# Optimization experiments

Measured on AMD Instinct MI355X. Metric: run time of the kernel, lower is better.

The kernel has to match this reference:

```python
import jax, jax.numpy as jnp
import numpy as np

B = 131072     # batch of observations
OBS = 17       # HalfCheetah-v5 obs dim
ACT = 6        # HalfCheetah-v5 action dim
M = 16         # number of charts / experts
HID = 256      # encoder / value hidden width (hardcoded in module)
GHID = 128     # gate hidden width (hardcoded)
R = 24.0       # chart radius in whitened feature space
BETA = 1.0     # locality prior strength
NEG = -1e9     # masked-logit fill (finite to keep grads clean)
LOG_STD_MIN, LOG_STD_MAX = -20.0, 2.0


def setup_inputs() -> dict:
    key = jax.random.key(0)
    ks = jax.random.split(key, 12)
    def rn(i, shape, sc):
        return jax.random.normal(ks[i], shape, dtype=jnp.float32) * sc
    return {
        "obs": jax.random.normal(ks[0], (B, OBS), dtype=jnp.float32),
        # encoder MLP (only the two hidden tanh layers feed the feature 'feat')
        "W1": rn(1, (OBS, HID), 0.2), "b1": jnp.zeros((HID,), jnp.float32),
        "W2": rn(2, (HID, HID), 0.06), "b2": jnp.zeros((HID,), jnp.float32),
        # gate: Linear(256,128) -> tanh -> Linear(128,m)
        "Wg1": rn(3, (HID, GHID), 0.06), "bg1": jnp.zeros((GHID,), jnp.float32),
        "Wg2": rn(4, (GHID, M), 0.1), "bg2": jnp.zeros((M,), jnp.float32),
        # m local Gaussian heads: mu Linear(256, act), shared log_std param per head
        "muW": rn(5, (M, HID, ACT), 0.06), "mub": jnp.zeros((M, ACT), jnp.float32),
        "log_std": jnp.zeros((M, ACT), jnp.float32),
        # value head: 256 -> 256 -> 256 -> 1 with tanh
        "Wv1": rn(6, (HID, HID), 0.06), "bv1": jnp.zeros((HID,), jnp.float32),
        "Wv2": rn(7, (HID, HID), 0.06), "bv2": jnp.zeros((HID,), jnp.float32),
        "Wv3": rn(8, (HID, 1), 0.06), "bv3": jnp.zeros((1,), jnp.float32),
        # chart cover state (frozen params in the torch module)
        "centers": jax.random.normal(ks[9], (M, HID), dtype=jnp.float32),
        "stats_mean": jnp.zeros((HID,), jnp.float32),
        "stats_var": jnp.ones((HID,), jnp.float32),
    }


def reference(obs, W1, b1, W2, b2, Wg1, bg1, Wg2, bg2, muW, mub, log_std,
              Wv1, bv1, Wv2, bv2, Wv3, bv3, centers, stats_mean, stats_var):
    # shared encoder phi(o): two tanh layers -> feat [B, HID]
    feat = jnp.tanh(jnp.tanh(obs @ W1 + b1) @ W2 + b2)

    # whitened features and squared distances to chart centers (cdist via gram trick)
    zw = (feat - stats_mean) / jnp.sqrt(stats_var + 1e-6)          # [B, HID]
    d2 = jnp.maximum(
        jnp.sum(zw * zw, axis=-1, keepdims=True)
        + jnp.sum(centers * centers, axis=-1)
        - 2.0 * (zw @ centers.T), 0.0)                              # [B, M]
    dists = jnp.sqrt(d2)

    # gate logits + locality prior -beta * ||z - c_i||^2 / r^2
    logits = jnp.tanh(feat @ Wg1 + bg1) @ Wg2 + bg2 - BETA * d2 / (R * R)

    # masked softmax restricted to active charts; nearest chart always active
    active = dists <= R
    nearest = jax.nn.one_hot(jnp.argmin(dists, axis=1), M, dtype=bool)
    active = active | nearest
    g = jax.nn.softmax(jnp.where(active, logits, NEG), axis=1)      # [B, M]

    # local expert heads mu_i(z), then convex combination of mu and log_std
    mus = jnp.einsum('bd,mda->bma', feat, muW) + mub                # [B, M, ACT]
    mu_bar = jnp.einsum('bm,bma->ba', g, mus)                       # [B, ACT]
    s_bar = jnp.clip(g @ log_std, LOG_STD_MIN, LOG_STD_MAX)         # [B, ACT]

    # value head on shared features
    v = (jnp.tanh(jnp.tanh(feat @ Wv1 + bv1) @ Wv2 + bv2) @ Wv3 + bv3)[:, 0]
    return mu_bar, s_bar, v
```

## Files before the change

kernel.cpp:

```cpp
#include <hip/hip_runtime.h>
#include <hip/hip_bf16.h>

#define BDIM 512
#define TB 64
#define OBS_D 17
#define HID 256
#define GHID 128
#define NM 16
#define NACT 6

typedef __attribute__((ext_vector_type(8))) short short8;
typedef __attribute__((ext_vector_type(4))) float f32x4;

#define OFF_W1P    0u
#define OFF_W2P    16384u
#define OFF_WG1P   147456u
#define OFF_WG2P   212992u
#define OFF_CP     217088u
#define OFF_MUWP   225280u
#define OFF_WV1P   274432u
#define OFF_WV2P   405504u
#define OFF_CNORM  536576u
#define OFF_CCONST 536640u

__device__ __forceinline__ float tanh_fast(float x){
  float e = __expf(2.f * x);
  return fmaf(-2.f, __builtin_amdgcn_rcpf(e + 1.f), 1.f);
}
__device__ __forceinline__ short bf16b(float x){
  __hip_bfloat16 h = __float2bfloat16(x);
  return *reinterpret_cast<short*>(&h);
}

__global__ void prep_kernel(const float* __restrict__ W1, const float* __restrict__ W2,
    const float* __restrict__ Wg1, const float* __restrict__ Wg2,
    const float* __restrict__ muW, const float* __restrict__ Wv1, const float* __restrict__ Wv2,
    const float* __restrict__ centers, const float* __restrict__ smean, const float* __restrict__ svar,
    char* __restrict__ ws)
{
  __hip_bfloat16* w1p  = (__hip_bfloat16*)(ws + OFF_W1P);
  __hip_bfloat16* w2p  = (__hip_bfloat16*)(ws + OFF_W2P);
  __hip_bfloat16* wg1p = (__hip_bfloat16*)(ws + OFF_WG1P);
  __hip_bfloat16* wg2p = (__hip_bfloat16*)(ws + OFF_WG2P);
  __hip_bfloat16* cp   = (__hip_bfloat16*)(ws + OFF_CP);
  __hip_bfloat16* muwp = (__hip_bfloat16*)(ws + OFF_MUWP);
  __hip_bfloat16* wv1p = (__hip_bfloat16*)(ws + OFF_WV1P);
  __hip_bfloat16* wv2p = (__hip_bfloat16*)(ws + OFF_WV2P);
  float* cnorm  = (float*)(ws + OFF_CNORM);
  float* cconst = (float*)(ws + OFF_CCONST);

  int gid = blockIdx.x * blockDim.x + threadIdx.x;
  if (gid < NM){
    float s = 0.f; const float* c = centers + gid * HID;
    for (int k = 0; k < HID; ++k) s += c[k] * c[k];
    cnorm[gid] = s;
  } else if (gid < 2*NM){
    int m = gid - NM; float s = 0.f; const float* c = centers + m * HID;
    for (int k = 0; k < HID; ++k) s += smean[k] * rsqrtf(svar[k] + 1e-6f) * c[k];
    cconst[m] = s;
  }

  const int T0 = 8192, T1 = T0+65536, T2 = T1+32768, T3 = T2+2048,
            T4 = T3+4096, T5 = T4+24576, T6 = T5+65536, T7 = T6+65536;
  for (int i = gid; i < T7; i += gridDim.x * blockDim.x){
    float v; __hip_bfloat16* dst;
    if (i < T0){ int idx=i;    int kb8=idx/(256*8); int n=(idx/8)%256; int e=idx&7; int k=kb8*8+e;
      v = (k < OBS_D) ? W1[k*256+n] : 0.f; dst = &w1p[idx]; }
    else if (i < T1){ int idx=i-T0; int kb8=idx/(256*8); int n=(idx/8)%256; int e=idx&7; int k=kb8*8+e;
      v = W2[k*256+n]; dst = &w2p[idx]; }
    else if (i < T2){ int idx=i-T1; int kb8=idx/(128*8); int n=(idx/8)%128; int e=idx&7; int k=kb8*8+e;
      v = Wg1[k*128+n]; dst = &wg1p[idx]; }
    else if (i < T3){ int idx=i-T2; int kb8=idx/(16*8);  int n=(idx/8)%16;  int e=idx&7; int k=kb8*8+e;
      v = Wg2[k*16+n]; dst = &wg2p[idx]; }
    else if (i < T4){ int idx=i-T3; int kb8=idx/(16*8);  int m=(idx/8)%16;  int e=idx&7; int k=kb8*8+e;
      v = centers[m*HID+k] * rsqrtf(svar[k] + 1e-6f); dst = &cp[idx]; }
    else if (i < T5){ int idx=i-T4; int kb8=idx/(96*8);  int n=(idx/8)%96;  int e=idx&7; int k=kb8*8+e;
      int a = n >> 4, m = n & 15;
      v = muW[m*(HID*NACT) + k*NACT + a]; dst = &muwp[idx]; }
    else if (i < T6){ int idx=i-T5; int kb8=idx/(256*8); int n=(idx/8)%256; int e=idx&7; int k=kb8*8+e;
      v = Wv1[k*256+n]; dst = &wv1p[idx]; }
    else            { int idx=i-T6; int kb8=idx/(256*8); int n=(idx/8)%256; int e=idx&7; int k=kb8*8+e;
      v = Wv2[k*256+n]; dst = &wv2p[idx]; }
    *dst = __float2bfloat16(v);
  }
}

__global__ __launch_bounds__(BDIM, 4) void moe_kernel(
  const float* __restrict__ obs,
  const float* __restrict__ b1, const float* __restrict__ b2,
  const float* __restrict__ bg1, const float* __restrict__ bg2,
  const float* __restrict__ mub, const float* __restrict__ lstd,
  const float* __restrict__ bv1, const float* __restrict__ bv2,
  const float* __restrict__ Wv3, const float* __restrict__ bv3,
  const float* __restrict__ smean, const float* __restrict__ svar,
  const char* __restrict__ ws, float* __restrict__ out, int Btot)
{
  const short8* w1p  = (const short8*)(ws + OFF_W1P);
  const short8* w2p  = (const short8*)(ws + OFF_W2P);
  const short8* wg1p = (const short8*)(ws + OFF_WG1P);
  const short8* wg2p = (const short8*)(ws + OFF_WG2P);
  const short8* cp   = (const short8*)(ws + OFF_CP);
  const short8* muwp = (const short8*)(ws + OFF_MUWP);
  const short8* wv1p = (const short8*)(ws + OFF_WV1P);
  const short8* wv2p = (const short8*)(ws + OFF_WV2P);
  const float* cnorm  = (const float*)(ws + OFF_CNORM);
  const float* cconst = (const float*)(ws + OFF_CCONST);

  const int tid = threadIdx.x;
  const int w = tid >> 6, lane = tid & 63, l16 = lane & 15, lk = lane >> 4;
  const int rowg0 = blockIdx.x * TB;

  __shared__ __hip_bfloat16 feat_s[32*64*8];
  __shared__ __hip_bfloat16 sc_s[32*64*8];
  __shared__ float part_s[8][64];
  __shared__ float g_s[64*17];

  short8 aO[4];
  #pragma unroll
  for (int rt = 0; rt < 4; ++rt){
    const float* orow = obs + (size_t)(rowg0 + rt*16 + l16) * OBS_D;
    #pragma unroll
    for (int e = 0; e < 8; ++e){ int k = lk*8 + e; float v = (k < OBS_D) ? orow[k] : 0.f; aO[rt][e] = bf16b(v); }
  }

  #pragma unroll
  for (int ctl = 0; ctl < 2; ++ctl){
    const int ct = w*2 + ctl;
    short8 B = w1p[lk*256 + ct*16 + l16];
    const int col = ct*16 + l16; const float bb = b1[col];
    #pragma unroll
    for (int rt = 0; rt < 4; ++rt){
      f32x4 acc = {0.f,0.f,0.f,0.f};
      acc = __builtin_amdgcn_mfma_f32_16x16x32_bf16(aO[rt], B, acc, 0,0,0);
      #pragma unroll
      for (int r = 0; r < 4; ++r){
        int row = rt*16 + lk*4 + r;
        sc_s[((col>>3)*64 + row)*8 + (col&7)] = __float2bfloat16(tanh_fast(acc[r] + bb));
      }
    }
  }
  __syncthreads();

  {
    f32x4 acc2[2][4];
    #pragma unroll
    for (int i = 0; i < 2; ++i)
      #pragma unroll
      for (int j = 0; j < 4; ++j) acc2[i][j] = (f32x4){0.f,0.f,0.f,0.f};
    #pragma unroll
    for (int ck = 0; ck < 8; ++ck){
      short8 A[4];
      #pragma unroll
      for (int rt = 0; rt < 4; ++rt) A[rt] = *(const short8*)&sc_s[((ck*4+lk)*64 + rt*16 + l16)*8];
      #pragma unroll
      for (int ctl = 0; ctl < 2; ++ctl){
        short8 B = w2p[(ck*4+lk)*256 + (w*2+ctl)*16 + l16];
        #pragma unroll
        for (int rt = 0; rt < 4; ++rt)
          acc2[ctl][rt] = __builtin_amdgcn_mfma_f32_16x16x32_bf16(A[rt], B, acc2[ctl][rt], 0,0,0);
      }
    }
    float znp[16];
    #pragma unroll
    for (int i = 0; i < 16; ++i) znp[i] = 0.f;
    #pragma unroll
    for (int ctl = 0; ctl < 2; ++ctl){
      const int col = (w*2+ctl)*16 + l16;
      const float bb = b2[col], mn = smean[col], iv = rsqrtf(svar[col] + 1e-6f);
      #pragma unroll
      for (int rt = 0; rt < 4; ++rt){
        #pragma unroll
        for (int r = 0; r < 4; ++r){
          int row = rt*16 + lk*4 + r;
          float tf = tanh_fast(acc2[ctl][rt][r] + bb);
          feat_s[((col>>3)*64 + row)*8 + (col&7)] = __float2bfloat16(tf);
          float z = (tf - mn) * iv;
          znp[rt*4+r] += z * z;
        }
      }
    }
    #pragma unroll
    for (int d = 1; d < 16; d <<= 1){
      #pragma unroll
      for (int i = 0; i < 16; ++i) znp[i] += __shfl_xor(znp[i], d, 64);
    }
    if (l16 == 0){
      #pragma unroll
      for (int i = 0; i < 16; ++i) part_s[w][(i>>2)*16 + lk*4 + (i&3)] = znp[i];
    }
  }
  __syncthreads();

  f32x4 accD = {0.f,0.f,0.f,0.f};
  {
    f32x4 acc3[4];
    #pragma unroll
    for (int j = 0; j < 4; ++j) acc3[j] = (f32x4){0.f,0.f,0.f,0.f};
    #pragma unroll
    for (int ck = 0; ck < 8; ++ck){
      short8 A[4];
      #pragma unroll
      for (int rt = 0; rt < 4; ++rt) A[rt] = *(const short8*)&feat_s[((ck*4+lk)*64 + rt*16 + l16)*8];
      if (w < 4)
        accD = __builtin_amdgcn_mfma_f32_16x16x32_bf16(A[w], cp[(ck*4+lk)*16 + l16], accD, 0,0,0);
      short8 B = wg1p[(ck*4+lk)*128 + w*16 + l16];
      #pragma unroll
      for (int rt = 0; rt < 4; ++rt)
        acc3[rt] = __builtin_amdgcn_mfma_f32_16x16x32_bf16(A[rt], B, acc3[rt], 0,0,0);
    }
    const int col = w*16 + l16;
    const float bb = bg1[col];
    #pragma unroll
    for (int rt = 0; rt < 4; ++rt)
      #pragma unroll
      for (int r = 0; r < 4; ++r){
        int row = rt*16 + lk*4 + r;
        sc_s[((col>>3)*64 + row)*8 + (col&7)] = __float2bfloat16(tanh_fast(acc3[rt][r] + bb));
      }
  }
  __syncthreads();

  if (w < 4){
    const int rw = w*16;
    f32x4 accL = {0.f,0.f,0.f,0.f};
    #pragma unroll
    for (int ks = 0; ks < 4; ++ks){
      short8 aT = *(const short8*)&sc_s[((ks*4+lk)*64 + rw + l16)*8];
      accL = __builtin_amdgcn_mfma_f32_16x16x32_bf16(aT, wg2p[(ks*4+lk)*16 + l16], accL, 0,0,0);
    }
    const float cn = cnorm[l16], cc = cconst[l16], bg2v = bg2[l16];
    float gw[4];
    #pragma unroll
    for (int r = 0; r < 4; ++r){
      int rowl = rw + lk*4 + r;
      float znr = 0.f;
      #pragma unroll
      for (int i = 0; i < 8; ++i) znr += part_s[i][rowl];
      float dot = accD[r] - cc;
      float d2 = fmaxf(znr + cn - 2.f*dot, 0.f);
      float lg = accL[r] + bg2v - d2 * (1.f/576.f);
      float mv = d2; int mi = l16;
      #pragma unroll
      for (int d = 1; d < 16; d <<= 1){
        float ov = __shfl_xor(mv, d, 64); int oi = __shfl_xor(mi, d, 64);
        if (ov < mv || (ov == mv && oi < mi)){ mv = ov; mi = oi; }
      }
      bool act = (d2 <= 576.f) || (mi == l16);
      lg = act ? lg : -1e9f;
      float mx = lg;
      #pragma unroll
      for (int d = 1; d < 16; d <<= 1) mx = fmaxf(mx, __shfl_xor(mx, d, 64));
      float ev = __expf(lg - mx);
      float sm = ev;
      #pragma unroll
      for (int d = 1; d < 16; d <<= 1) sm += __shfl_xor(sm, d, 64);
      gw[r] = ev * __builtin_amdgcn_rcpf(sm);
      g_s[rowl*17 + l16] = gw[r];
    }
    #pragma unroll
    for (int r = 0; r < 4; ++r){
      float sb[6];
      #pragma unroll
      for (int a = 0; a < 6; ++a) sb[a] = gw[r] * lstd[l16*6 + a];
      #pragma unroll
      for (int d = 1; d < 16; d <<= 1){
        #pragma unroll
        for (int a = 0; a < 6; ++a) sb[a] += __shfl_xor(sb[a], d, 64);
      }
      if (l16 == 0){
        int row = rowg0 + rw + lk*4 + r;
        #pragma unroll
        for (int a = 0; a < 6; ++a)
          out[(size_t)6*Btot + (size_t)row*6 + a] = fminf(fmaxf(sb[a], -20.f), 2.f);
      }
    }
  } else {
    f32x4 acc7[2][4];
    #pragma unroll
    for (int i = 0; i < 2; ++i)
      #pragma unroll
      for (int j = 0; j < 4; ++j) acc7[i][j] = (f32x4){0.f,0.f,0.f,0.f};
    #pragma unroll
    for (int ck = 0; ck < 8; ++ck){
      short8 A[4];
      #pragma unroll
      for (int rt = 0; rt < 4; ++rt) A[rt] = *(const short8*)&feat_s[((ck*4+lk)*64 + rt*16 + l16)*8];
      #pragma unroll
      for (int ctl = 0; ctl < 2; ++ctl){
        short8 B = wv1p[(ck*4+lk)*256 + (8 + (w-4)*2 + ctl)*16 + l16];
        #pragma unroll
        for (int rt = 0; rt < 4; ++rt)
          acc7[ctl][rt] = __builtin_amdgcn_mfma_f32_16x16x32_bf16(A[rt], B, acc7[ctl][rt], 0,0,0);
      }
    }
    #pragma unroll
    for (int ctl = 0; ctl < 2; ++ctl){
      const int col = (8 + (w-4)*2 + ctl)*16 + l16;
      const float bb = bv1[col];
      #pragma unroll
      for (int rt = 0; rt < 4; ++rt)
        #pragma unroll
        for (int r = 0; r < 4; ++r){
          int row = rt*16 + lk*4 + r;
          sc_s[((col>>3)*64 + row)*8 + (col&7)] = __float2bfloat16(tanh_fast(acc7[ctl][rt][r] + bb));
        }
    }
  }
  __syncthreads();

  if (w < 4){
    f32x4 acc7[2][4];
    #pragma unroll
    for (int i = 0; i < 2; ++i)
      #pragma unroll
      for (int j = 0; j < 4; ++j) acc7[i][j] = (f32x4){0.f,0.f,0.f,0.f};
    #pragma unroll
    for (int ck = 0; ck < 8; ++ck){
      short8 A[4];
      #pragma unroll
      for (int rt = 0; rt < 4; ++rt) A[rt] = *(const short8*)&feat_s[((ck*4+lk)*64 + rt*16 + l16)*8];
      #pragma unroll
      for (int ctl = 0; ctl < 2; ++ctl){
        short8 B = wv1p[(ck*4+lk)*256 + (w*2 + ctl)*16 + l16];
        #pragma unroll
        for (int rt = 0; rt < 4; ++rt)
          acc7[ctl][rt] = __builtin_amdgcn_mfma_f32_16x16x32_bf16(A[rt], B, acc7[ctl][rt], 0,0,0);
      }
    }
    #pragma unroll
    for (int ctl = 0; ctl < 2; ++ctl){
      const int col = (w*2 + ctl)*16 + l16;
      const float bb = bv1[col];
      #pragma unroll
      for (int rt = 0; rt < 4; ++rt)
        #pragma unroll
        for (int r = 0; r < 4; ++r){
          int row = rt*16 + lk*4 + r;
          sc_s[((col>>3)*64 + row)*8 + (col&7)] = __float2bfloat16(tanh_fast(acc7[ctl][rt][r] + bb));
        }
    }
  } else {
    const int na = (w < 6) ? 2 : 1;
    const int a0 = (w < 6) ? (w-4)*2 : (w-2);
    f32x4 accM[2][4];
    #pragma unroll
    for (int i = 0; i < 2; ++i)
      #pragma unroll
      for (int j = 0; j < 4; ++j) accM[i][j] = (f32x4){0.f,0.f,0.f,0.f};
    #pragma unroll
    for (int ck = 0; ck < 8; ++ck){
      short8 A[4];
      #pragma unroll
      for (int rt = 0; rt < 4; ++rt) A[rt] = *(const short8*)&feat_s[((ck*4+lk)*64 + rt*16 + l16)*8];
      #pragma unroll
      for (int al = 0; al < 2; ++al){
        if (al < na){
          short8 B = muwp[(ck*4+lk)*96 + (a0+al)*16 + l16];
          #pragma unroll
          for (int rt = 0; rt < 4; ++rt)
            accM[al][rt] = __builtin_amdgcn_mfma_f32_16x16x32_bf16(A[rt], B, accM[al][rt], 0,0,0);
        }
      }
    }
    #pragma unroll
    for (int al = 0; al < 2; ++al){
      if (al < na){
        const int a = a0 + al;
        const float mubv = mub[l16*6 + a];
        #pragma unroll
        for (int rt = 0; rt < 4; ++rt){
          #pragma unroll
          for (int r = 0; r < 4; ++r){
            int row = rt*16 + lk*4 + r;
            float m = (accM[al][rt][r] + mubv) * g_s[row*17 + l16];
            #pragma unroll
            for (int d = 1; d < 16; d <<= 1) m += __shfl_xor(m, d, 64);
            if (l16 == 0) out[(size_t)(rowg0 + row)*6 + a] = m;
          }
        }
      }
    }
  }
  __syncthreads();

  {
    f32x4 acc8[2][4];
    #pragma unroll
    for (int i = 0; i < 2; ++i)
      #pragma unroll
      for (int j = 0; j < 4; ++j) acc8[i][j] = (f32x4){0.f,0.f,0.f,0.f};
    #pragma unroll
    for (int ck = 0; ck < 8; ++ck){
      short8 A[4];
      #pragma unroll
      for (int rt = 0; rt < 4; ++rt) A[rt] = *(const short8*)&sc_s[((ck*4+lk)*64 + rt*16 + l16)*8];
      #pragma unroll
      for (int ctl = 0; ctl < 2; ++ctl){
        short8 B = wv2p[(ck*4+lk)*256 + (w*2+ctl)*16 + l16];
        #pragma unroll
        for (int rt = 0; rt < 4; ++rt)
          acc8[ctl][rt] = __builtin_amdgcn_mfma_f32_16x16x32_bf16(A[rt], B, acc8[ctl][rt], 0,0,0);
      }
    }
    float vpp[16];
    #pragma unroll
    for (int i = 0; i < 16; ++i) vpp[i] = 0.f;
    #pragma unroll
    for (int ctl = 0; ctl < 2; ++ctl){
      const int col = (w*2+ctl)*16 + l16;
      const float bb = bv2[col], w3 = Wv3[col];
      #pragma unroll
      for (int rt = 0; rt < 4; ++rt)
        #pragma unroll
        for (int r = 0; r < 4; ++r)
          vpp[rt*4+r] += tanh_fast(acc8[ctl][rt][r] + bb) * w3;
    }
    #pragma unroll
    for (int d = 1; d < 16; d <<= 1){
      #pragma unroll
      for (int i = 0; i < 16; ++i) vpp[i] += __shfl_xor(vpp[i], d, 64);
    }
    if (l16 == 0){
      #pragma unroll
      for (int i = 0; i < 16; ++i) part_s[w][(i>>2)*16 + lk*4 + (i&3)] = vpp[i];
    }
  }
  __syncthreads();
  if (tid < 64){
    float v = bv3[0];
    #pragma unroll
    for (int i = 0; i < 8; ++i) v += part_s[i][tid];
    out[(size_t)12*Btot + rowg0 + tid] = v;
  }
}

extern "C" void kernel_launch(void* const* d_in, const int* in_sizes, int n_in,
                              void* d_out, int out_size, void* d_ws, size_t ws_size,
                              hipStream_t stream){
  const float* obs = (const float*)d_in[0];
  const float* W1  = (const float*)d_in[1];  const float* b1  = (const float*)d_in[2];
  const float* W2  = (const float*)d_in[3];  const float* b2  = (const float*)d_in[4];
  const float* Wg1 = (const float*)d_in[5];  const float* bg1 = (const float*)d_in[6];
  const float* Wg2 = (const float*)d_in[7];  const float* bg2 = (const float*)d_in[8];
  const float* muW = (const float*)d_in[9];  const float* mub = (const float*)d_in[10];
  const float* lstd= (const float*)d_in[11];
  const float* Wv1 = (const float*)d_in[12]; const float* bv1 = (const float*)d_in[13];
  const float* Wv2 = (const float*)d_in[14]; const float* bv2 = (const float*)d_in[15];
  const float* Wv3 = (const float*)d_in[16]; const float* bv3 = (const float*)d_in[17];
  const float* centers = (const float*)d_in[18];
  const float* smean   = (const float*)d_in[19];
  const float* svar    = (const float*)d_in[20];
  int Btot = in_sizes[0] / OBS_D;
  char* ws = (char*)d_ws;

  hipLaunchKernelGGL(prep_kernel, dim3(512), dim3(256), 0, stream,
      W1, W2, Wg1, Wg2, muW, Wv1, Wv2, centers, smean, svar, ws);
  hipLaunchKernelGGL(moe_kernel, dim3(Btot / TB), dim3(BDIM), 0, stream,
      obs, b1, b2, bg1, bg2, mub, lstd, bv1, bv2, Wv3, bv3, smean, svar,
      (const char*)ws, (float*)d_out, Btot);
}
```

Before: 209.2 us.

## Retile warps into 2x4 row-by-column grid for all MFMA stages

Instead of each of the 8 waves covering all 64 rows and a narrow slice of columns, the waves are arranged as 2 row-groups by 4 column-groups, each handling 32 rows and wider column slices. This halves the per-wave LDS A-fragment reads and enlarges the reuse of each global weight fragment across more MFMAs. The gate/value/mu work split and the partial-sum reductions are re-indexed to match. The mu head now uses two waves with three actions each, so no wave sits idle. The change may shift register pressure and the balance between global weight loads and LDS reads.

```diff
diff --git a/kernel.cpp b/kernel.cpp
--- a/kernel.cpp
+++ b/kernel.cpp
@@ -108,33 +108,35 @@
 
   const int tid = threadIdx.x;
   const int w = tid >> 6, lane = tid & 63, l16 = lane & 15, lk = lane >> 4;
+  const int wr = w >> 2, wc = w & 3;
   const int rowg0 = blockIdx.x * TB;
+  const int rbase = wr * 32;
 
   __shared__ __hip_bfloat16 feat_s[32*64*8];
   __shared__ __hip_bfloat16 sc_s[32*64*8];
   __shared__ float part_s[8][64];
   __shared__ float g_s[64*17];
 
-  short8 aO[4];
+  short8 aO[2];
   #pragma unroll
-  for (int rt = 0; rt < 4; ++rt){
-    const float* orow = obs + (size_t)(rowg0 + rt*16 + l16) * OBS_D;
+  for (int rt = 0; rt < 2; ++rt){
+    const float* orow = obs + (size_t)(rowg0 + rbase + rt*16 + l16) * OBS_D;
     #pragma unroll
     for (int e = 0; e < 8; ++e){ int k = lk*8 + e; float v = (k < OBS_D) ? orow[k] : 0.f; aO[rt][e] = bf16b(v); }
   }
 
   #pragma unroll
-  for (int ctl = 0; ctl < 2; ++ctl){
-    const int ct = w*2 + ctl;
+  for (int ctl = 0; ctl < 4; ++ctl){
+    const int ct = wc*4 + ctl;
     short8 B = w1p[lk*256 + ct*16 + l16];
     const int col = ct*16 + l16; const float bb = b1[col];
     #pragma unroll
-    for (int rt = 0; rt < 4; ++rt){
+    for (int rt = 0; rt < 2; ++rt){
       f32x4 acc = {0.f,0.f,0.f,0.f};
       acc = __builtin_amdgcn_mfma_f32_16x16x32_bf16(aO[rt], B, acc, 0,0,0);
       #pragma unroll
       for (int r = 0; r < 4; ++r){
-        int row = rt*16 + lk*4 + r;
+        int row = rbase + rt*16 + lk*4 + r;
         sc_s[((col>>3)*64 + row)*8 + (col&7)] = __float2bfloat16(tanh_fast(acc[r] + bb));
       }
     }
@@ -142,36 +144,36 @@
   __syncthreads();
 
   {
-    f32x4 acc2[2][4];
-    #pragma unroll
-    for (int i = 0; i < 2; ++i)
-      #pragma unroll
-      for (int j = 0; j < 4; ++j) acc2[i][j] = (f32x4){0.f,0.f,0.f,0.f};
-    #pragma unroll
-    for (int ck = 0; ck < 8; ++ck){
-      short8 A[4];
-      #pragma unroll
-      for (int rt = 0; rt < 4; ++rt) A[rt] = *(const short8*)&sc_s[((ck*4+lk)*64 + rt*16 + l16)*8];
-      #pragma unroll
-      for (int ctl = 0; ctl < 2; ++ctl){
-        short8 B = w2p[(ck*4+lk)*256 + (w*2+ctl)*16 + l16];
-        #pragma unroll
-        for (int rt = 0; rt < 4; ++rt)
+    f32x4 acc2[4][2];
+    #pragma unroll
+    for (int i = 0; i < 4; ++i)
+      #pragma unroll
+      for (int j = 0; j < 2; ++j) acc2[i][j] = (f32x4){0.f,0.f,0.f,0.f};
+    #pragma unroll
+    for (int ck = 0; ck < 8; ++ck){
+      short8 A[2];
+      #pragma unroll
+      for (int rt = 0; rt < 2; ++rt) A[rt] = *(const short8*)&sc_s[((ck*4+lk)*64 + rbase + rt*16 + l16)*8];
+      #pragma unroll
+      for (int ctl = 0; ctl < 4; ++ctl){
+        short8 B = w2p[(ck*4+lk)*256 + (wc*4+ctl)*16 + l16];
+        #pragma unroll
+        for (int rt = 0; rt < 2; ++rt)
           acc2[ctl][rt] = __builtin_amdgcn_mfma_f32_16x16x32_bf16(A[rt], B, acc2[ctl][rt], 0,0,0);
       }
     }
-    float znp[16];
-    #pragma unroll
-    for (int i = 0; i < 16; ++i) znp[i] = 0.f;
-    #pragma unroll
-    for (int ctl = 0; ctl < 2; ++ctl){
-      const int col = (w*2+ctl)*16 + l16;
+    float znp[8];
+    #pragma unroll
+    for (int i = 0; i < 8; ++i) znp[i] = 0.f;
+    #pragma unroll
+    for (int ctl = 0; ctl < 4; ++ctl){
+      const int col = (wc*4+ctl)*16 + l16;
       const float bb = b2[col], mn = smean[col], iv = rsqrtf(svar[col] + 1e-6f);
       #pragma unroll
-      for (int rt = 0; rt < 4; ++rt){
+      for (int rt = 0; rt < 2; ++rt){
         #pragma unroll
         for (int r = 0; r < 4; ++r){
-          int row = rt*16 + lk*4 + r;
+          int row = rbase + rt*16 + lk*4 + r;
           float tf = tanh_fast(acc2[ctl][rt][r] + bb);
           feat_s[((col>>3)*64 + row)*8 + (col&7)] = __float2bfloat16(tf);
           float z = (tf - mn) * iv;
@@ -182,46 +184,54 @@
     #pragma unroll
     for (int d = 1; d < 16; d <<= 1){
       #pragma unroll
-      for (int i = 0; i < 16; ++i) znp[i] += __shfl_xor(znp[i], d, 64);
+      for (int i = 0; i < 8; ++i) znp[i] += __shfl_xor(znp[i], d, 64);
     }
     if (l16 == 0){
       #pragma unroll
-      for (int i = 0; i < 16; ++i) part_s[w][(i>>2)*16 + lk*4 + (i&3)] = znp[i];
+      for (int i = 0; i < 8; ++i) part_s[w][rbase + (i>>2)*16 + lk*4 + (i&3)] = znp[i];
     }
   }
   __syncthreads();
 
   f32x4 accD = {0.f,0.f,0.f,0.f};
   {
-    f32x4 acc3[4];
-    #pragma unroll
-    for (int j = 0; j < 4; ++j) acc3[j] = (f32x4){0.f,0.f,0.f,0.f};
-    #pragma unroll
-    for (int ck = 0; ck < 8; ++ck){
-      short8 A[4];
-      #pragma unroll
-      for (int rt = 0; rt < 4; ++rt) A[rt] = *(const short8*)&feat_s[((ck*4+lk)*64 + rt*16 + l16)*8];
-      if (w < 4)
-        accD = __builtin_amdgcn_mfma_f32_16x16x32_bf16(A[w], cp[(ck*4+lk)*16 + l16], accD, 0,0,0);
-      short8 B = wg1p[(ck*4+lk)*128 + w*16 + l16];
-      #pragma unroll
-      for (int rt = 0; rt < 4; ++rt)
-        acc3[rt] = __builtin_amdgcn_mfma_f32_16x16x32_bf16(A[rt], B, acc3[rt], 0,0,0);
-    }
-    const int col = w*16 + l16;
-    const float bb = bg1[col];
-    #pragma unroll
-    for (int rt = 0; rt < 4; ++rt)
-      #pragma unroll
-      for (int r = 0; r < 4; ++r){
-        int row = rt*16 + lk*4 + r;
-        sc_s[((col>>3)*64 + row)*8 + (col&7)] = __float2bfloat16(tanh_fast(acc3[rt][r] + bb));
-      }
-  }
-  __syncthreads();
-
-  if (w < 4){
-    const int rw = w*16;
+    f32x4 acc3[2][2];
+    #pragma unroll
+    for (int i = 0; i < 2; ++i)
+      #pragma unroll
+      for (int j = 0; j < 2; ++j) acc3[i][j] = (f32x4){0.f,0.f,0.f,0.f};
+    #pragma unroll
+    for (int ck = 0; ck < 8; ++ck){
+      short8 A[2];
+      #pragma unroll
+      for (int rt = 0; rt < 2; ++rt) A[rt] = *(const short8*)&feat_s[((ck*4+lk)*64 + rbase + rt*16 + l16)*8];
+      if (wc < 2)
+        accD = __builtin_amdgcn_mfma_f32_16x16x32_bf16(A[wc], cp[(ck*4+lk)*16 + l16], accD, 0,0,0);
+      #pragma unroll
+      for (int ctl = 0; ctl < 2; ++ctl){
+        short8 B = wg1p[(ck*4+lk)*128 + (wc*2+ctl)*16 + l16];
+        #pragma unroll
+        for (int rt = 0; rt < 2; ++rt)
+          acc3[ctl][rt] = __builtin_amdgcn_mfma_f32_16x16x32_bf16(A[rt], B, acc3[ctl][rt], 0,0,0);
+      }
+    }
+    #pragma unroll
+    for (int ctl = 0; ctl < 2; ++ctl){
+      const int col = (wc*2+ctl)*16 + l16;
+      const float bb = bg1[col];
+      #pragma unroll
+      for (int rt = 0; rt < 2; ++rt)
+        #pragma unroll
+        for (int r = 0; r < 4; ++r){
+          int row = rbase + rt*16 + lk*4 + r;
+          sc_s[((col>>3)*64 + row)*8 + (col&7)] = __float2bfloat16(tanh_fast(acc3[ctl][rt][r] + bb));
+        }
+    }
+  }
+  __syncthreads();
+
+  if (wc < 2){
+    const int rw = rbase + wc*16;
     f32x4 accL = {0.f,0.f,0.f,0.f};
     #pragma unroll
     for (int ks = 0; ks < 4; ++ks){
@@ -233,9 +243,8 @@
     #pragma unroll
     for (int r = 0; r < 4; ++r){
       int rowl = rw + lk*4 + r;
-      float znr = 0.f;
-      #pragma unroll
-      for (int i = 0; i < 8; ++i) znr += part_s[i][rowl];
+      float znr = part_s[wr*4+0][rowl] + part_s[wr*4+1][rowl]
+                + part_s[wr*4+2][rowl] + part_s[wr*4+3][rowl];
       float dot = accD[r] - cc;
       float d2 = fmaxf(znr + cn - 2.f*dot, 0.f);
       float lg = accL[r] + bg2v - d2 * (1.f/576.f);
@@ -275,142 +284,136 @@
       }
     }
   } else {
-    f32x4 acc7[2][4];
-    #pragma unroll
-    for (int i = 0; i < 2; ++i)
-      #pragma unroll
-      for (int j = 0; j < 4; ++j) acc7[i][j] = (f32x4){0.f,0.f,0.f,0.f};
-    #pragma unroll
-    for (int ck = 0; ck < 8; ++ck){
-      short8 A[4];
-      #pragma unroll
-      for (int rt = 0; rt < 4; ++rt) A[rt] = *(const short8*)&feat_s[((ck*4+lk)*64 + rt*16 + l16)*8];
-      #pragma unroll
-      for (int ctl = 0; ctl < 2; ++ctl){
-        short8 B = wv1p[(ck*4+lk)*256 + (8 + (w-4)*2 + ctl)*16 + l16];
-        #pragma unroll
-        for (int rt = 0; rt < 4; ++rt)
+    f32x4 acc7[4][2];
+    #pragma unroll
+    for (int i = 0; i < 4; ++i)
+      #pragma unroll
+      for (int j = 0; j < 2; ++j) acc7[i][j] = (f32x4){0.f,0.f,0.f,0.f};
+    #pragma unroll
+    for (int ck = 0; ck < 8; ++ck){
+      short8 A[2];
+      #pragma unroll
+      for (int rt = 0; rt < 2; ++rt) A[rt] = *(const short8*)&feat_s[((ck*4+lk)*64 + rbase + rt*16 + l16)*8];
+      #pragma unroll
+      for (int ctl = 0; ctl < 4; ++ctl){
+        short8 B = wv1p[(ck*4+lk)*256 + (8 + (wc-2)*4 + ctl)*16 + l16];
+        #pragma unroll
+        for (int rt = 0; rt < 2; ++rt)
           acc7[ctl][rt] = __builtin_amdgcn_mfma_f32_16x16x32_bf16(A[rt], B, acc7[ctl][rt], 0,0,0);
       }
     }
     #pragma unroll
-    for (int ctl = 0; ctl < 2; ++ctl){
-      const int col = (8 + (w-4)*2 + ctl)*16 + l16;
+    for (int ctl = 0; ctl < 4; ++ctl){
+      const int col = (8 + (wc-2)*4 + ctl)*16 + l16;
       const float bb = bv1[col];
       #pragma unroll
-      for (int rt = 0; rt < 4; ++rt)
+      for (int rt = 0; rt < 2; ++rt)
         #pragma unroll
         for (int r = 0; r < 4; ++r){
-          int row = rt*16 + lk*4 + r;
+          int row = rbase + rt*16 + lk*4 + r;
           sc_s[((col>>3)*64 + row)*8 + (col&7)] = __float2bfloat16(tanh_fast(acc7[ctl][rt][r] + bb));
         }
     }
   }
   __syncthreads();
 
-  if (w < 4){
-    f32x4 acc7[2][4];
-    #pragma unroll
-    for (int i = 0; i < 2; ++i)
-      #pragma unroll
-      for (int j = 0; j < 4; ++j) acc7[i][j] = (f32x4){0.f,0.f,0.f,0.f};
-    #pragma unroll
-    for (int ck = 0; ck < 8; ++ck){
-      short8 A[4];
-      #pragma unroll
-      for (int rt = 0; rt < 4; ++rt) A[rt] = *(const short8*)&feat_s[((ck*4+lk)*64 + rt*16 + l16)*8];
-      #pragma unroll
-      for (int ctl = 0; ctl < 2; ++ctl){
-        short8 B = wv1p[(ck*4+lk)*256 + (w*2 + ctl)*16 + l16];
-        #pragma unroll
-        for (int rt = 0; rt < 4; ++rt)
+  if (wc < 2){
+    f32x4 acc7[4][2];
+    #pragma unroll
+    for (int i = 0; i < 4; ++i)
+      #pragma unroll
+      for (int j = 0; j < 2; ++j) acc7[i][j] = (f32x4){0.f,0.f,0.f,0.f};
+    #pragma unroll
+    for (int ck = 0; ck < 8; ++ck){
+      short8 A[2];
+      #pragma unroll
+      for (int rt = 0; rt < 2; ++rt) A[rt] = *(const short8*)&feat_s[((ck*4+lk)*64 + rbase + rt*16 + l16)*8];
+      #pragma unroll
+      for (int ctl = 0; ctl < 4; ++ctl){
+        short8 B = wv1p[(ck*4+lk)*256 + (wc*4 + ctl)*16 + l16];
+        #pragma unroll
+        for (int rt = 0; rt < 2; ++rt)
           acc7[ctl][rt] = __builtin_amdgcn_mfma_f32_16x16x32_bf16(A[rt], B, acc7[ctl][rt], 0,0,0);
       }
     }
     #pragma unroll
-    for (int ctl = 0; ctl < 2; ++ctl){
-      const int col = (w*2 + ctl)*16 + l16;
+    for (int ctl = 0; ctl < 4; ++ctl){
+      const int col = (wc*4 + ctl)*16 + l16;
       const float bb = bv1[col];
       #pragma unroll
-      for (int rt = 0; rt < 4; ++rt)
+      for (int rt = 0; rt < 2; ++rt)
         #pragma unroll
         for (int r = 0; r < 4; ++r){
-          int row = rt*16 + lk*4 + r;
+          int row = rbase + rt*16 + lk*4 + r;
           sc_s[((col>>3)*64 + row)*8 + (col&7)] = __float2bfloat16(tanh_fast(acc7[ctl][rt][r] + bb));
         }
     }
   } else {
-    const int na = (w < 6) ? 2 : 1;
-    const int a0 = (w < 6) ? (w-4)*2 : (w-2);
-    f32x4 accM[2][4];
-    #pragma unroll
-    for (int i = 0; i < 2; ++i)
-      #pragma unroll
-      for (int j = 0; j < 4; ++j) accM[i][j] = (f32x4){0.f,0.f,0.f,0.f};
-    #pragma unroll
-    for (int ck = 0; ck < 8; ++ck){
-      short8 A[4];
-      #pragma unroll
-      for (int rt = 0; rt < 4; ++rt) A[rt] = *(const short8*)&feat_s[((ck*4+lk)*64 + rt*16 + l16)*8];
-      #pragma unroll
-      for (int al = 0; al < 2; ++al){
-        if (al < na){
-          short8 B = muwp[(ck*4+lk)*96 + (a0+al)*16 + l16];
+    f32x4 accM[3][2];
+    #pragma unroll
+    for (int i = 0; i < 3; ++i)
+      #pragma unroll
+      for (int j = 0; j < 2; ++j) accM[i][j] = (f32x4){0.f,0.f,0.f,0.f};
+    #pragma unroll
+    for (int ck = 0; ck < 8; ++ck){
+      short8 A[2];
+      #pragma unroll
+      for (int rt = 0; rt < 2; ++rt) A[rt] = *(const short8*)&feat_s[((ck*4+lk)*64 + rbase + rt*16 + l16)*8];
+      #pragma unroll
+      for (int al = 0; al < 3; ++al){
+        short8 B = muwp[(ck*4+lk)*96 + ((wc-2)*3 + al)*16 + l16];
+        #pragma unroll
+        for (int rt = 0; rt < 2; ++rt)
+          accM[al][rt] = __builtin_amdgcn_mfma_f32_16x16x32_bf16(A[rt], B, accM[al][rt], 0,0,0);
+      }
+    }
+    #pragma unroll
+    for (int al = 0; al < 3; ++al){
+      const int a = (wc-2)*3 + al;
+      const float mubv = mub[l16*6 + a];
+      #pragma unroll
+      for (int rt = 0; rt < 2; ++rt){
+        #pragma unroll
+        for (int r = 0; r < 4; ++r){
+          int row = rbase + rt*16 + lk*4 + r;
+          float m = (accM[al][rt][r] + mubv) * g_s[row*17 + l16];
           #pragma unroll
-          for (int rt = 0; rt < 4; ++rt)
-            accM[al][rt] = __builtin_amdgcn_mfma_f32_16x16x32_bf16(A[rt], B, accM[al][rt], 0,0,0);
+          for (int d = 1; d < 16; d <<= 1) m += __shfl_xor(m, d, 64);
+          if (l16 == 0) out[(size_t)(rowg0 + row)*6 + a] = m;
         }
       }
     }
-    #pragma unroll
-    for (int al = 0; al < 2; ++al){
-      if (al < na){
-        const int a = a0 + al;
-        const float mubv = mub[l16*6 + a];
-        #pragma unroll
-        for (int rt = 0; rt < 4; ++rt){
-          #pragma unroll
-          for (int r = 0; r < 4; ++r){
-            int row = rt*16 + lk*4 + r;
-            float m = (accM[al][rt][r] + mubv) * g_s[row*17 + l16];
-            #pragma unroll
-            for (int d = 1; d < 16; d <<= 1) m += __shfl_xor(m, d, 64);
-            if (l16 == 0) out[(size_t)(rowg0 + row)*6 + a] = m;
-          }
-        }
-      }
-    }
   }
   __syncthreads();
 
   {
-    f32x4 acc8[2][4];
-    #pragma unroll
-    for (int i = 0; i < 2; ++i)
-      #pragma unroll
-      for (int j = 0; j < 4; ++j) acc8[i][j] = (f32x4){0.f,0.f,0.f,0.f};
-    #pragma unroll
-    for (int ck = 0; ck < 8; ++ck){
-      short8 A[4];
-      #pragma unroll
-      for (int rt = 0; rt < 4; ++rt) A[rt] = *(const short8*)&sc_s[((ck*4+lk)*64 + rt*16 + l16)*8];
-      #pragma unroll
-      for (int ctl = 0; ctl < 2; ++ctl){
-        short8 B = wv2p[(ck*4+lk)*256 + (w*2+ctl)*16 + l16];
-        #pragma unroll
-        for (int rt = 0; rt < 4; ++rt)
+    f32x4 acc8[4][2];
+    #pragma unroll
+    for (int i = 0; i < 4; ++i)
+      #pragma unroll
+      for (int j = 0; j < 2; ++j) acc8[i][j] = (f32x4){0.f,0.f,0.f,0.f};
+    #pragma unroll
+    for (int ck = 0; ck < 8; ++ck){
+      short8 A[2];
+      #pragma unroll
+      for (int rt = 0; rt < 2; ++rt) A[rt] = *(const short8*)&sc_s[((ck*4+lk)*64 + rbase + rt*16 + l16)*8];
+      #pragma unroll
+      for (int ctl = 0; ctl < 4; ++ctl){
+        short8 B = wv2p[(ck*4+lk)*256 + (wc*4+ctl)*16 + l16];
+        #pragma unroll
+        for (int rt = 0; rt < 2; ++rt)
           acc8[ctl][rt] = __builtin_amdgcn_mfma_f32_16x16x32_bf16(A[rt], B, acc8[ctl][rt], 0,0,0);
       }
     }
-    float vpp[16];
-    #pragma unroll
-    for (int i = 0; i < 16; ++i) vpp[i] = 0.f;
-    #pragma unroll
-    for (int ctl = 0; ctl < 2; ++ctl){
-      const int col = (w*2+ctl)*16 + l16;
+    float vpp[8];
+    #pragma unroll
+    for (int i = 0; i < 8; ++i) vpp[i] = 0.f;
+    #pragma unroll
+    for (int ctl = 0; ctl < 4; ++ctl){
+      const int col = (wc*4+ctl)*16 + l16;
       const float bb = bv2[col], w3 = Wv3[col];
       #pragma unroll
-      for (int rt = 0; rt < 4; ++rt)
+      for (int rt = 0; rt < 2; ++rt)
         #pragma unroll
         for (int r = 0; r < 4; ++r)
           vpp[rt*4+r] += tanh_fast(acc8[ctl][rt][r] + bb) * w3;
@@ -418,18 +421,18 @@
     #pragma unroll
     for (int d = 1; d < 16; d <<= 1){
       #pragma unroll
-      for (int i = 0; i < 16; ++i) vpp[i] += __shfl_xor(vpp[i], d, 64);
+      for (int i = 0; i < 8; ++i) vpp[i] += __shfl_xor(vpp[i], d, 64);
     }
     if (l16 == 0){
       #pragma unroll
-      for (int i = 0; i < 16; ++i) part_s[w][(i>>2)*16 + lk*4 + (i&3)] = vpp[i];
+      for (int i = 0; i < 8; ++i) part_s[w][rbase + (i>>2)*16 + lk*4 + (i&3)] = vpp[i];
     }
   }
   __syncthreads();
   if (tid < 64){
-    float v = bv3[0];
-    #pragma unroll
-    for (int i = 0; i < 8; ++i) v += part_s[i][tid];
+    int g = tid >> 5;
+    float v = part_s[g*4+0][tid] + part_s[g*4+1][tid]
+            + part_s[g*4+2][tid] + part_s[g*4+3][tid] + bv3[0];
     out[(size_t)12*Btot + rowg0 + tid] = v;
   }
 }
```

Result: faster. 185.4 us (-11.4%).
